# Kernel optimization log

Hardware: AMD Instinct MI355X
Metric: run time of the kernel (lower is better)

Reference implementation:

```python
import jax, jax.numpy as jnp
import numpy as np

N = 100000      # nodes
E = 1600000     # edges
IN, HG, HM, OUT = 512, 64, 64, 20


def _glorot(key, fan_in, fan_out):
    lim = 1.0 / np.sqrt(fan_in)
    return jax.random.uniform(key, (fan_in, fan_out), jnp.float32, -lim, lim)


def setup_inputs() -> dict:
    key = jax.random.key(0)
    ks = jax.random.split(key, 16)
    inp = {
        "x": jax.random.normal(ks[0], (N, IN), jnp.float32),
        "edge_index": jax.random.randint(ks[1], (2, E), 0, N, jnp.int64),
        "edge_attrs": jax.random.uniform(ks[2], (E,), jnp.float32),
        # GCNConv weights (PyG: x @ W then aggregate, + bias)
        "gc0_w": _glorot(ks[3], IN, HG), "gc0_b": jnp.zeros((HG,), jnp.float32),
        "gc1_w": _glorot(ks[4], HG, HG), "gc1_b": jnp.zeros((HG,), jnp.float32),
        "lin0_w": _glorot(ks[5], HG, HM), "lin0_b": jnp.zeros((HM,), jnp.float32),
        "lin1_w": _glorot(ks[6], HM, HM), "lin1_b": jnp.zeros((HM,), jnp.float32),
        "lin2_w": _glorot(ks[7], HM, HM), "lin2_b": jnp.zeros((HM,), jnp.float32),
        "lin3_w": _glorot(ks[8], HM, OUT), "lin3_b": jnp.zeros((OUT,), jnp.float32),
    }
    return inp


def _gcn_norm(edge_index, edge_attrs):
    # Add self loops (weight 1), compute symmetric normalization D^-1/2 A D^-1/2
    loop = jnp.arange(N, dtype=edge_index.dtype)
    row = jnp.concatenate([edge_index[0], loop])
    col = jnp.concatenate([edge_index[1], loop])
    w = jnp.concatenate([edge_attrs, jnp.ones((N,), edge_attrs.dtype)])
    deg = jax.ops.segment_sum(w, col, num_segments=N)
    dinv = jnp.where(deg > 0, jax.lax.rsqrt(jnp.maximum(deg, 1e-30)), 0.0)
    norm = dinv[row] * w * dinv[col]
    return row, col, norm


def _gcn_conv(x, W, b, row, col, norm):
    xw = x @ W                                   # [N, H]
    msg = norm[:, None] * xw[row]                # [E+N, H]
    return jax.ops.segment_sum(msg, col, num_segments=N) + b


def reference(x, edge_index, edge_attrs,
              gc0_w, gc0_b, gc1_w, gc1_b,
              lin0_w, lin0_b, lin1_w, lin1_b, lin2_w, lin2_b, lin3_w, lin3_b):
    row, col, norm = _gcn_norm(edge_index, edge_attrs)
    h = jax.nn.selu(_gcn_conv(x, gc0_w, gc0_b, row, col, norm))
    h = jax.nn.selu(_gcn_conv(h, gc1_w, gc1_b, row, col, norm))
    h = jax.nn.selu(h @ lin0_w + lin0_b)
    h = jax.nn.selu(h @ lin1_w + lin1_b)
    h = jax.nn.selu(h @ lin2_w + lin2_b)
    return jax.nn.softmax(h @ lin3_w + lin3_b, axis=-1)
```

## Files before the change

kernel.cpp:

```cpp
#include <hip/hip_runtime.h>
#include <math.h>

#define IN_DIM 512
#define HG 64
#define OUT_DIM 20

typedef __attribute__((ext_vector_type(8))) short bf16x8;
typedef __attribute__((ext_vector_type(4))) float f32x4;

__device__ __forceinline__ float selu_f(float x) {
    const float a = 1.6732632423543772f;
    const float s = 1.0507009873554805f;
    return x > 0.f ? s * x : s * a * expm1f(x);
}

__device__ __forceinline__ unsigned short f2bf(float f) {
    unsigned int u = __float_as_uint(f);
    u += 0x7FFFu + ((u >> 16) & 1u);
    return (unsigned short)(u >> 16);
}
__device__ __forceinline__ float bf2f(unsigned short b) {
    return __uint_as_float(((unsigned int)b) << 16);
}


__global__ void k_init(float* deg, int* cnt, int n) {
    int i = blockIdx.x * 256 + threadIdx.x;
    if (i < n) { deg[i] = 1.0f; cnt[i] = 0; }
}

__global__ void k_edgedeg(const int* __restrict__ ei, const float* __restrict__ ea,
                          float* deg, int* cnt, int E) {
    int e = blockIdx.x * 256 + threadIdx.x;
    if (e >= E) return;
    int c = ei[E + e];
    atomicAdd(&deg[c], ea[e]);
    atomicAdd(&cnt[c], 1);
}

__global__ void k_rsqrt(float* deg, int n) {
    int i = blockIdx.x * 256 + threadIdx.x;
    if (i < n) { float d = deg[i]; deg[i] = d > 0.f ? 1.0f / sqrtf(d) : 0.f; }
}

__device__ __forceinline__ int block_excl_scan(int v, int tid, int* wsum, int nw, int* total_out) {
    int lane = tid & 63, wv = tid >> 6;
    int incl = v;
    #pragma unroll
    for (int s = 1; s < 64; s <<= 1) {
        int t = __shfl_up(incl, s, 64);
        if (lane >= s) incl += t;
    }
    if (lane == 63) wsum[wv] = incl;
    __syncthreads();
    int prefix = 0;
    for (int i = 0; i < wv; i++) prefix += wsum[i];
    int total = 0;
    for (int i = 0; i < nw; i++) total += wsum[i];
    *total_out = total;
    return prefix + incl - v;
}

__global__ void k_scan1(const int* __restrict__ cnt, int* __restrict__ offar,
                        int* __restrict__ blockSums, int n) {
    __shared__ int wsum[4];
    int i = blockIdx.x * 256 + threadIdx.x;
    int v = (i < n) ? cnt[i] : 0;
    int total;
    int excl = block_excl_scan(v, threadIdx.x, wsum, 4, &total);
    if (i < n) offar[i] = excl;
    if (threadIdx.x == 0) blockSums[blockIdx.x] = total;
}

__global__ void k_scan2(const int* __restrict__ blockSums, int* __restrict__ blockOffs, int nb) {
    __shared__ int wsum[8];
    int v = (threadIdx.x < nb) ? blockSums[threadIdx.x] : 0;
    int total;
    int excl = block_excl_scan(v, threadIdx.x, wsum, 8, &total);
    if (threadIdx.x < nb) blockOffs[threadIdx.x] = excl;
}

__global__ void k_scan3(int* __restrict__ offar, const int* __restrict__ blockOffs,
                        int* __restrict__ cursor, int n, int E) {
    int i = blockIdx.x * 256 + threadIdx.x;
    if (i < n) {
        int o = offar[i] + blockOffs[blockIdx.x];
        offar[i] = o;
        cursor[i] = o;
    }
    if (i == 0) offar[n] = E;
}

__global__ void k_scatter(const int* __restrict__ ei, const float* __restrict__ ea,
                          const float* __restrict__ dinv, int* cursor,
                          int* __restrict__ srcA, float* __restrict__ valA, int E) {
    int e = blockIdx.x * 256 + threadIdx.x;
    if (e >= E) return;
    int r = ei[e], c = ei[E + e];
    int pos = atomicAdd(&cursor[c], 1);
    srcA[pos] = r;
    valA[pos] = dinv[r] * ea[e] * dinv[c];
}


__global__ void k_splitw(const float* __restrict__ W, unsigned short* __restrict__ hi,
                         unsigned short* __restrict__ lo, int K, int C, int Cpad) {
    int i = blockIdx.x * 256 + threadIdx.x;
    if (i >= Cpad * K) return;
    int c = i / K, k = i - c * K;
    float wv = (c < C) ? W[(size_t)k * C + c] : 0.f;
    unsigned short h = f2bf(wv);
    hi[i] = h;
    lo[i] = f2bf(wv - bf2f(h));
}


template <int K, bool BIAS, bool ACT>
__global__ __launch_bounds__(256, 3)
void k_gemm_mfma(const float* __restrict__ A, const unsigned short* __restrict__ WThi,
                 const unsigned short* __restrict__ WTlo, const float* __restrict__ bias,
                 float* __restrict__ out, int n) {
    const int t = threadIdx.x;
    const int lane = t & 63;
    const int w = t >> 6;
    const int l15 = lane & 15;
    const int g = lane >> 4;
    const int r0 = blockIdx.x * 128 + w * 32;
    if (r0 >= n) return;

    f32x4 acc[2][4];
    #pragma unroll
    for (int rt = 0; rt < 2; rt++)
        #pragma unroll
        for (int ct = 0; ct < 4; ct++) acc[rt][ct] = (f32x4)0.f;

    #pragma unroll 1
    for (int k0 = 0; k0 < K; k0 += 32) {
        bf16x8 bh[4], bl[4];
        #pragma unroll
        for (int ct = 0; ct < 4; ct++) {
            size_t off = (size_t)(ct * 16 + l15) * K + k0 + 8 * g;
            bh[ct] = *(const bf16x8*)(WThi + off);
            bl[ct] = *(const bf16x8*)(WTlo + off);
        }
        #pragma unroll
        for (int rt = 0; rt < 2; rt++) {
            const float* ap = A + (size_t)(r0 + rt * 16 + l15) * K + k0 + 8 * g;
            float4 v0 = *(const float4*)(ap);
            float4 v1 = *(const float4*)(ap + 4);
            float vv[8] = {v0.x, v0.y, v0.z, v0.w, v1.x, v1.y, v1.z, v1.w};
            bf16x8 ah, al;
            #pragma unroll
            for (int j = 0; j < 8; j++) {
                unsigned short h = f2bf(vv[j]);
                ah[j] = (short)h;
                al[j] = (short)f2bf(vv[j] - bf2f(h));
            }
            #pragma unroll
            for (int ct = 0; ct < 4; ct++) {
                acc[rt][ct] = __builtin_amdgcn_mfma_f32_16x16x32_bf16(ah, bh[ct], acc[rt][ct], 0, 0, 0);
                acc[rt][ct] = __builtin_amdgcn_mfma_f32_16x16x32_bf16(ah, bl[ct], acc[rt][ct], 0, 0, 0);
                acc[rt][ct] = __builtin_amdgcn_mfma_f32_16x16x32_bf16(al, bh[ct], acc[rt][ct], 0, 0, 0);
            }
        }
    }

    float bv[4];
    #pragma unroll
    for (int ct = 0; ct < 4; ct++) bv[ct] = BIAS ? bias[ct * 16 + l15] : 0.f;

    #pragma unroll
    for (int rt = 0; rt < 2; rt++) {
        #pragma unroll
        for (int r = 0; r < 4; r++) {
            int gr = r0 + rt * 16 + 4 * g + r;
            #pragma unroll
            for (int ct = 0; ct < 4; ct++) {
                float v = acc[rt][ct][r] + bv[ct];
                if (ACT) v = selu_f(v);
                out[(size_t)gr * 64 + ct * 16 + l15] = v;
            }
        }
    }
}


__global__ __launch_bounds__(256, 3)
void k_lin3s(const float* __restrict__ A, const unsigned short* __restrict__ WThi,
             const unsigned short* __restrict__ WTlo, const float* __restrict__ b3,
             float* __restrict__ out, int n) {
    const int t = threadIdx.x;
    const int lane = t & 63;
    const int w = t >> 6;
    const int l15 = lane & 15;
    const int g = lane >> 4;
    const int r0 = blockIdx.x * 128 + w * 32;
    if (r0 >= n) return;

    f32x4 acc[2][2];
    #pragma unroll
    for (int rt = 0; rt < 2; rt++)
        #pragma unroll
        for (int ct = 0; ct < 2; ct++) acc[rt][ct] = (f32x4)0.f;

    #pragma unroll 1
    for (int k0 = 0; k0 < 64; k0 += 32) {
        bf16x8 bh[2], bl[2];
        #pragma unroll
        for (int ct = 0; ct < 2; ct++) {
            size_t off = (size_t)(ct * 16 + l15) * 64 + k0 + 8 * g;
            bh[ct] = *(const bf16x8*)(WThi + off);
            bl[ct] = *(const bf16x8*)(WTlo + off);
        }
        #pragma unroll
        for (int rt = 0; rt < 2; rt++) {
            const float* ap = A + (size_t)(r0 + rt * 16 + l15) * 64 + k0 + 8 * g;
            float4 v0 = *(const float4*)(ap);
            float4 v1 = *(const float4*)(ap + 4);
            float vv[8] = {v0.x, v0.y, v0.z, v0.w, v1.x, v1.y, v1.z, v1.w};
            bf16x8 ah, al;
            #pragma unroll
            for (int j = 0; j < 8; j++) {
                unsigned short h = f2bf(vv[j]);
                ah[j] = (short)h;
                al[j] = (short)f2bf(vv[j] - bf2f(h));
            }
            #pragma unroll
            for (int ct = 0; ct < 2; ct++) {
                acc[rt][ct] = __builtin_amdgcn_mfma_f32_16x16x32_bf16(ah, bh[ct], acc[rt][ct], 0, 0, 0);
                acc[rt][ct] = __builtin_amdgcn_mfma_f32_16x16x32_bf16(ah, bl[ct], acc[rt][ct], 0, 0, 0);
                acc[rt][ct] = __builtin_amdgcn_mfma_f32_16x16x32_bf16(al, bh[ct], acc[rt][ct], 0, 0, 0);
            }
        }
    }

    float b0v = b3[l15];
    float b1v = (l15 < 4) ? b3[16 + l15] : 0.f;

    #pragma unroll
    for (int rt = 0; rt < 2; rt++) {
        #pragma unroll
        for (int r = 0; r < 4; r++) {
            int gr = r0 + rt * 16 + 4 * g + r;
            float v0 = acc[rt][0][r] + b0v;
            float v1 = (l15 < 4) ? acc[rt][1][r] + b1v : -INFINITY;
            float mx = fmaxf(v0, v1);
            mx = fmaxf(mx, __shfl_xor(mx, 1));
            mx = fmaxf(mx, __shfl_xor(mx, 2));
            mx = fmaxf(mx, __shfl_xor(mx, 4));
            mx = fmaxf(mx, __shfl_xor(mx, 8));
            float e0 = expf(v0 - mx);
            float e1 = (l15 < 4) ? expf(v1 - mx) : 0.f;
            float s = e0 + e1;
            s += __shfl_xor(s, 1);
            s += __shfl_xor(s, 2);
            s += __shfl_xor(s, 4);
            s += __shfl_xor(s, 8);
            float inv = 1.0f / s;
            out[(size_t)gr * OUT_DIM + l15] = e0 * inv;
            if (l15 < 4) out[(size_t)gr * OUT_DIM + 16 + l15] = e1 * inv;
        }
    }
}


__global__ __launch_bounds__(256) void k_agg(const float* __restrict__ xw, const float* __restrict__ dinv,
                                             const int* __restrict__ off, const int* __restrict__ srcA,
                                             const float* __restrict__ valA, const float* __restrict__ bias,
                                             float* __restrict__ out, int n) {
    int node = (blockIdx.x * 256 + threadIdx.x) >> 6;
    int lane = threadIdx.x & 63;
    if (node >= n) return;
    float d = dinv[node];
    float acc = d * d * xw[(size_t)node * 64 + lane];
    int p0 = off[node], p1 = off[node + 1];
    for (int p = p0; p < p1; ++p) {
        int s = srcA[p];
        float v = valA[p];
        acc += v * xw[(size_t)s * 64 + lane];
    }
    out[(size_t)node * 64 + lane] = selu_f(acc + bias[lane]);
}


extern "C" void kernel_launch(void* const* d_in, const int* in_sizes, int n_in,
                              void* d_out, int out_size, void* d_ws, size_t ws_size,
                              hipStream_t stream) {
    const float* x     = (const float*)d_in[0];
    const int*   ei    = (const int*)d_in[1];
    const float* ea    = (const float*)d_in[2];
    const float* gc0_w = (const float*)d_in[3];
    const float* gc0_b = (const float*)d_in[4];
    const float* gc1_w = (const float*)d_in[5];
    const float* gc1_b = (const float*)d_in[6];
    const float* lin0_w = (const float*)d_in[7];
    const float* lin0_b = (const float*)d_in[8];
    const float* lin1_w = (const float*)d_in[9];
    const float* lin1_b = (const float*)d_in[10];
    const float* lin2_w = (const float*)d_in[11];
    const float* lin2_b = (const float*)d_in[12];
    const float* lin3_w = (const float*)d_in[13];
    const float* lin3_b = (const float*)d_in[14];
    float* out = (float*)d_out;

    const int N = in_sizes[0] / IN_DIM;
    const int E = in_sizes[2];
    const int nb1 = (N + 255) / 256;

    char* w = (char*)d_ws;
    auto alloc = [&](size_t bytes) { char* p = w; w += (bytes + 255) & ~(size_t)255; return p; };
    float* dinv      = (float*)alloc((size_t)N * 4);
    int*   cnt       = (int*)alloc((size_t)N * 4);
    int*   offar     = (int*)alloc((size_t)(N + 1) * 4);
    int*   cursor    = (int*)alloc((size_t)N * 4);
    int*   blockSums = (int*)alloc((size_t)nb1 * 4);
    int*   blockOffs = (int*)alloc((size_t)nb1 * 4);
    int*   srcA      = (int*)alloc((size_t)E * 4);
    float* valA      = (float*)alloc((size_t)E * 4);
    float* bufA      = (float*)alloc((size_t)N * 64 * 4);
    float* bufB      = (float*)alloc((size_t)N * 64 * 4);
    unsigned short* wt0h = (unsigned short*)alloc(64 * 512 * 2);
    unsigned short* wt0l = (unsigned short*)alloc(64 * 512 * 2);
    unsigned short* wt1h = (unsigned short*)alloc(64 * 64 * 2);
    unsigned short* wt1l = (unsigned short*)alloc(64 * 64 * 2);
    unsigned short* wl0h = (unsigned short*)alloc(64 * 64 * 2);
    unsigned short* wl0l = (unsigned short*)alloc(64 * 64 * 2);
    unsigned short* wl1h = (unsigned short*)alloc(64 * 64 * 2);
    unsigned short* wl1l = (unsigned short*)alloc(64 * 64 * 2);
    unsigned short* wl2h = (unsigned short*)alloc(64 * 64 * 2);
    unsigned short* wl2l = (unsigned short*)alloc(64 * 64 * 2);
    unsigned short* wt3h = (unsigned short*)alloc(32 * 64 * 2);
    unsigned short* wt3l = (unsigned short*)alloc(32 * 64 * 2);

    const int gN = (N + 255) / 256;
    const int gE = (E + 255) / 256;
    const int gT = (N + 127) / 128;
    const int gA = (N + 3) / 4;

    k_init<<<gN, 256, 0, stream>>>(dinv, cnt, N);
    k_edgedeg<<<gE, 256, 0, stream>>>(ei, ea, dinv, cnt, E);
    k_rsqrt<<<gN, 256, 0, stream>>>(dinv, N);
    k_scan1<<<nb1, 256, 0, stream>>>(cnt, offar, blockSums, N);
    k_scan2<<<1, 512, 0, stream>>>(blockSums, blockOffs, nb1);
    k_scan3<<<nb1, 256, 0, stream>>>(offar, blockOffs, cursor, N, E);
    k_scatter<<<gE, 256, 0, stream>>>(ei, ea, dinv, cursor, srcA, valA, E);

    k_splitw<<<128, 256, 0, stream>>>(gc0_w, wt0h, wt0l, 512, 64, 64);
    k_splitw<<<16, 256, 0, stream>>>(gc1_w, wt1h, wt1l, 64, 64, 64);
    k_splitw<<<16, 256, 0, stream>>>(lin0_w, wl0h, wl0l, 64, 64, 64);
    k_splitw<<<16, 256, 0, stream>>>(lin1_w, wl1h, wl1l, 64, 64, 64);
    k_splitw<<<16, 256, 0, stream>>>(lin2_w, wl2h, wl2l, 64, 64, 64);
    k_splitw<<<8, 256, 0, stream>>>(lin3_w, wt3h, wt3l, 64, OUT_DIM, 32);

    k_gemm_mfma<IN_DIM, false, false><<<gT, 256, 0, stream>>>(x, wt0h, wt0l, nullptr, bufA, N);
    k_agg<<<gA, 256, 0, stream>>>(bufA, dinv, offar, srcA, valA, gc0_b, bufB, N);
    k_gemm_mfma<HG, false, false><<<gT, 256, 0, stream>>>(bufB, wt1h, wt1l, nullptr, bufA, N);
    k_agg<<<gA, 256, 0, stream>>>(bufA, dinv, offar, srcA, valA, gc1_b, bufB, N);
    k_gemm_mfma<HG, true, true><<<gT, 256, 0, stream>>>(bufB, wl0h, wl0l, lin0_b, bufA, N);
    k_gemm_mfma<HG, true, true><<<gT, 256, 0, stream>>>(bufA, wl1h, wl1l, lin1_b, bufB, N);
    k_gemm_mfma<HG, true, true><<<gT, 256, 0, stream>>>(bufB, wl2h, wl2l, lin2_b, bufA, N);
    k_lin3s<<<gT, 256, 0, stream>>>(bufA, wt3h, wt3l, lin3_b, out, N);
}
```

Measured before the change: 1.013 ms.

## Fuse dense MLP stack into one register-resident kernel; vectorize aggregation

The three hidden linear layers and the final linear+softmax are merged into one kernel. Activations stay in registers as split-bf16 MFMA operands, computed in transposed form so each layer's output feeds the next layer's B operand, which removes three round trips of a 100k×64 fp32 buffer through global memory. Separately, the aggregation kernel now has each wavefront handle a node with two half-waves over alternating edges, loading float2 per lane and unrolling by four to raise memory-level parallelism. The fused kernel adds register pressure, and the lin3 weight reads for padded rows 20-31 depend on how that buffer was sized.

```diff
diff --git a/kernel.cpp b/kernel.cpp
--- a/kernel.cpp
+++ b/kernel.cpp
@@ -6,6 +6,7 @@
 #define OUT_DIM 20
 
 typedef __attribute__((ext_vector_type(8))) short bf16x8;
+typedef __attribute__((ext_vector_type(4))) short bf16x4;
 typedef __attribute__((ext_vector_type(4))) float f32x4;
 
 __device__ __forceinline__ float selu_f(float x) {
@@ -185,85 +186,6 @@
 }
 
 
-__global__ __launch_bounds__(256, 3)
-void k_lin3s(const float* __restrict__ A, const unsigned short* __restrict__ WThi,
-             const unsigned short* __restrict__ WTlo, const float* __restrict__ b3,
-             float* __restrict__ out, int n) {
-    const int t = threadIdx.x;
-    const int lane = t & 63;
-    const int w = t >> 6;
-    const int l15 = lane & 15;
-    const int g = lane >> 4;
-    const int r0 = blockIdx.x * 128 + w * 32;
-    if (r0 >= n) return;
-
-    f32x4 acc[2][2];
-    #pragma unroll
-    for (int rt = 0; rt < 2; rt++)
-        #pragma unroll
-        for (int ct = 0; ct < 2; ct++) acc[rt][ct] = (f32x4)0.f;
-
-    #pragma unroll 1
-    for (int k0 = 0; k0 < 64; k0 += 32) {
-        bf16x8 bh[2], bl[2];
-        #pragma unroll
-        for (int ct = 0; ct < 2; ct++) {
-            size_t off = (size_t)(ct * 16 + l15) * 64 + k0 + 8 * g;
-            bh[ct] = *(const bf16x8*)(WThi + off);
-            bl[ct] = *(const bf16x8*)(WTlo + off);
-        }
-        #pragma unroll
-        for (int rt = 0; rt < 2; rt++) {
-            const float* ap = A + (size_t)(r0 + rt * 16 + l15) * 64 + k0 + 8 * g;
-            float4 v0 = *(const float4*)(ap);
-            float4 v1 = *(const float4*)(ap + 4);
-            float vv[8] = {v0.x, v0.y, v0.z, v0.w, v1.x, v1.y, v1.z, v1.w};
-            bf16x8 ah, al;
-            #pragma unroll
-            for (int j = 0; j < 8; j++) {
-                unsigned short h = f2bf(vv[j]);
-                ah[j] = (short)h;
-                al[j] = (short)f2bf(vv[j] - bf2f(h));
-            }
-            #pragma unroll
-            for (int ct = 0; ct < 2; ct++) {
-                acc[rt][ct] = __builtin_amdgcn_mfma_f32_16x16x32_bf16(ah, bh[ct], acc[rt][ct], 0, 0, 0);
-                acc[rt][ct] = __builtin_amdgcn_mfma_f32_16x16x32_bf16(ah, bl[ct], acc[rt][ct], 0, 0, 0);
-                acc[rt][ct] = __builtin_amdgcn_mfma_f32_16x16x32_bf16(al, bh[ct], acc[rt][ct], 0, 0, 0);
-            }
-        }
-    }
-
-    float b0v = b3[l15];
-    float b1v = (l15 < 4) ? b3[16 + l15] : 0.f;
-
-    #pragma unroll
-    for (int rt = 0; rt < 2; rt++) {
-        #pragma unroll
-        for (int r = 0; r < 4; r++) {
-            int gr = r0 + rt * 16 + 4 * g + r;
-            float v0 = acc[rt][0][r] + b0v;
-            float v1 = (l15 < 4) ? acc[rt][1][r] + b1v : -INFINITY;
-            float mx = fmaxf(v0, v1);
-            mx = fmaxf(mx, __shfl_xor(mx, 1));
-            mx = fmaxf(mx, __shfl_xor(mx, 2));
-            mx = fmaxf(mx, __shfl_xor(mx, 4));
-            mx = fmaxf(mx, __shfl_xor(mx, 8));
-            float e0 = expf(v0 - mx);
-            float e1 = (l15 < 4) ? expf(v1 - mx) : 0.f;
-            float s = e0 + e1;
-            s += __shfl_xor(s, 1);
-            s += __shfl_xor(s, 2);
-            s += __shfl_xor(s, 4);
-            s += __shfl_xor(s, 8);
-            float inv = 1.0f / s;
-            out[(size_t)gr * OUT_DIM + l15] = e0 * inv;
-            if (l15 < 4) out[(size_t)gr * OUT_DIM + 16 + l15] = e1 * inv;
-        }
-    }
-}
-
-
 __global__ __launch_bounds__(256) void k_agg(const float* __restrict__ xw, const float* __restrict__ dinv,
                                              const int* __restrict__ off, const int* __restrict__ srcA,
                                              const float* __restrict__ valA, const float* __restrict__ bias,
@@ -271,15 +193,196 @@
     int node = (blockIdx.x * 256 + threadIdx.x) >> 6;
     int lane = threadIdx.x & 63;
     if (node >= n) return;
-    float d = dinv[node];
-    float acc = d * d * xw[(size_t)node * 64 + lane];
+    const int half = lane >> 5;
+    const int l32 = lane & 31;
+    const float2* __restrict__ xw2 = (const float2*)xw;
+
     int p0 = off[node], p1 = off[node + 1];
-    for (int p = p0; p < p1; ++p) {
+    float ax = 0.f, ay = 0.f;
+    int p = p0 + half;
+    for (; p + 6 < p1; p += 8) {
+        int s0 = srcA[p];
+        int s1 = srcA[p + 2];
+        int s2 = srcA[p + 4];
+        int s3 = srcA[p + 6];
+        float v0 = valA[p], v1 = valA[p + 2], v2 = valA[p + 4], v3 = valA[p + 6];
+        float2 x0 = xw2[(size_t)s0 * 32 + l32];
+        float2 x1 = xw2[(size_t)s1 * 32 + l32];
+        float2 x2 = xw2[(size_t)s2 * 32 + l32];
+        float2 x3 = xw2[(size_t)s3 * 32 + l32];
+        ax += v0 * x0.x + v1 * x1.x + v2 * x2.x + v3 * x3.x;
+        ay += v0 * x0.y + v1 * x1.y + v2 * x2.y + v3 * x3.y;
+    }
+    for (; p < p1; p += 2) {
         int s = srcA[p];
         float v = valA[p];
-        acc += v * xw[(size_t)s * 64 + lane];
-    }
-    out[(size_t)node * 64 + lane] = selu_f(acc + bias[lane]);
+        float2 xv = xw2[(size_t)s * 32 + l32];
+        ax += v * xv.x;
+        ay += v * xv.y;
+    }
+    ax += __shfl_xor(ax, 32);
+    ay += __shfl_xor(ay, 32);
+    if (half == 0) {
+        float d = dinv[node];
+        float2 self = xw2[(size_t)node * 32 + l32];
+        float2 o;
+        o.x = selu_f(ax + d * d * self.x + bias[2 * l32]);
+        o.y = selu_f(ay + d * d * self.y + bias[2 * l32 + 1]);
+        ((float2*)out)[(size_t)node * 32 + l32] = o;
+    }
+}
+
+
+__global__ __launch_bounds__(256, 3)
+void k_dense(const float* __restrict__ H,
+             const unsigned short* __restrict__ w0h, const unsigned short* __restrict__ w0l, const float* __restrict__ b0,
+             const unsigned short* __restrict__ w1h, const unsigned short* __restrict__ w1l, const float* __restrict__ b1,
+             const unsigned short* __restrict__ w2h, const unsigned short* __restrict__ w2l, const float* __restrict__ b2,
+             const unsigned short* __restrict__ w3h, const unsigned short* __restrict__ w3l, const float* __restrict__ b3,
+             float* __restrict__ out, int n) {
+    const int t = threadIdx.x, lane = t & 63, w = t >> 6;
+    const int l15 = lane & 15, g = lane >> 4;
+    const int r0 = blockIdx.x * 128 + w * 32;
+    if (r0 >= n) return;
+
+    bf16x8 bh[2][2], bl[2][2];
+    #pragma unroll
+    for (int nt = 0; nt < 2; nt++) {
+        const float* hp = H + (size_t)(r0 + nt * 16 + l15) * 64;
+        #pragma unroll
+        for (int k0 = 0; k0 < 2; k0++) {
+            float4 c0 = *(const float4*)(hp + 32 * k0 + 4 * g);
+            float4 c1 = *(const float4*)(hp + 32 * k0 + 16 + 4 * g);
+            float vv[8] = {c0.x, c0.y, c0.z, c0.w, c1.x, c1.y, c1.z, c1.w};
+            #pragma unroll
+            for (int j = 0; j < 8; j++) {
+                unsigned short hb = f2bf(vv[j]);
+                bh[nt][k0][j] = (short)hb;
+                bl[nt][k0][j] = (short)f2bf(vv[j] - bf2f(hb));
+            }
+        }
+    }
+
+    const unsigned short* whs[3] = {w0h, w1h, w2h};
+    const unsigned short* wls[3] = {w0l, w1l, w2l};
+    const float* bs[3] = {b0, b1, b2};
+
+    #pragma unroll
+    for (int layer = 0; layer < 3; layer++) {
+        float accS[2][4][4];
+        #pragma unroll
+        for (int ct = 0; ct < 4; ct++) {
+            bf16x8 ah[2], al[2];
+            #pragma unroll
+            for (int k0 = 0; k0 < 2; k0++) {
+                size_t off = (size_t)(16 * ct + l15) * 64 + 32 * k0 + 4 * g;
+                bf16x4 h0 = *(const bf16x4*)(whs[layer] + off);
+                bf16x4 h1 = *(const bf16x4*)(whs[layer] + off + 16);
+                bf16x4 l0 = *(const bf16x4*)(wls[layer] + off);
+                bf16x4 l1 = *(const bf16x4*)(wls[layer] + off + 16);
+                #pragma unroll
+                for (int j = 0; j < 4; j++) {
+                    ah[k0][j] = h0[j]; ah[k0][4 + j] = h1[j];
+                    al[k0][j] = l0[j]; al[k0][4 + j] = l1[j];
+                }
+            }
+            float4 bv = *(const float4*)(bs[layer] + 16 * ct + 4 * g);
+            float bvr[4] = {bv.x, bv.y, bv.z, bv.w};
+            #pragma unroll
+            for (int nt = 0; nt < 2; nt++) {
+                f32x4 acc = (f32x4)0.f;
+                #pragma unroll
+                for (int k0 = 0; k0 < 2; k0++) {
+                    acc = __builtin_amdgcn_mfma_f32_16x16x32_bf16(ah[k0], bh[nt][k0], acc, 0, 0, 0);
+                    acc = __builtin_amdgcn_mfma_f32_16x16x32_bf16(ah[k0], bl[nt][k0], acc, 0, 0, 0);
+                    acc = __builtin_amdgcn_mfma_f32_16x16x32_bf16(al[k0], bh[nt][k0], acc, 0, 0, 0);
+                }
+                #pragma unroll
+                for (int r = 0; r < 4; r++) accS[nt][ct][r] = selu_f(acc[r] + bvr[r]);
+            }
+        }
+        #pragma unroll
+        for (int nt = 0; nt < 2; nt++)
+            #pragma unroll
+            for (int k0 = 0; k0 < 2; k0++)
+                #pragma unroll
+                for (int j = 0; j < 8; j++) {
+                    float v = accS[nt][2 * k0 + (j >> 2)][j & 3];
+                    unsigned short hb = f2bf(v);
+                    bh[nt][k0][j] = (short)hb;
+                    bl[nt][k0][j] = (short)f2bf(v - bf2f(hb));
+                }
+    }
+
+    float z[2][2][4];
+    #pragma unroll
+    for (int ct = 0; ct < 2; ct++) {
+        bf16x8 ah[2], al[2];
+        #pragma unroll
+        for (int k0 = 0; k0 < 2; k0++) {
+            size_t off = (size_t)(16 * ct + l15) * 64 + 32 * k0 + 4 * g;
+            bf16x4 h0 = *(const bf16x4*)(w3h + off);
+            bf16x4 h1 = *(const bf16x4*)(w3h + off + 16);
+            bf16x4 l0 = *(const bf16x4*)(w3l + off);
+            bf16x4 l1 = *(const bf16x4*)(w3l + off + 16);
+            #pragma unroll
+            for (int j = 0; j < 4; j++) {
+                ah[k0][j] = h0[j]; ah[k0][4 + j] = h1[j];
+                al[k0][j] = l0[j]; al[k0][4 + j] = l1[j];
+            }
+        }
+        #pragma unroll
+        for (int nt = 0; nt < 2; nt++) {
+            f32x4 acc = (f32x4)0.f;
+            #pragma unroll
+            for (int k0 = 0; k0 < 2; k0++) {
+                acc = __builtin_amdgcn_mfma_f32_16x16x32_bf16(ah[k0], bh[nt][k0], acc, 0, 0, 0);
+                acc = __builtin_amdgcn_mfma_f32_16x16x32_bf16(ah[k0], bl[nt][k0], acc, 0, 0, 0);
+                acc = __builtin_amdgcn_mfma_f32_16x16x32_bf16(al[k0], bh[nt][k0], acc, 0, 0, 0);
+            }
+            #pragma unroll
+            for (int r = 0; r < 4; r++) {
+                int f = 16 * ct + 4 * g + r;
+                float bb = (f < OUT_DIM) ? b3[f] : 0.f;
+                z[nt][ct][r] = acc[r] + bb;
+            }
+        }
+    }
+    #pragma unroll
+    for (int nt = 0; nt < 2; nt++) {
+        int node = r0 + nt * 16 + l15;
+        float mx = -INFINITY;
+        #pragma unroll
+        for (int ct = 0; ct < 2; ct++)
+            #pragma unroll
+            for (int r = 0; r < 4; r++) {
+                if (ct == 0 || g == 0) mx = fmaxf(mx, z[nt][ct][r]);
+            }
+        mx = fmaxf(mx, __shfl_xor(mx, 16));
+        mx = fmaxf(mx, __shfl_xor(mx, 32));
+        float e[2][4];
+        float s = 0.f;
+        #pragma unroll
+        for (int ct = 0; ct < 2; ct++)
+            #pragma unroll
+            for (int r = 0; r < 4; r++) {
+                if (ct == 0 || g == 0) {
+                    e[ct][r] = expf(z[nt][ct][r] - mx);
+                    s += e[ct][r];
+                } else e[ct][r] = 0.f;
+            }
+        s += __shfl_xor(s, 16);
+        s += __shfl_xor(s, 32);
+        float inv = 1.0f / s;
+        #pragma unroll
+        for (int ct = 0; ct < 2; ct++)
+            #pragma unroll
+            for (int r = 0; r < 4; r++) {
+                int f = 16 * ct + 4 * g + r;
+                if (ct == 0 || g == 0)
+                    out[(size_t)node * OUT_DIM + f] = e[ct][r] * inv;
+            }
+    }
 }
 
 
@@ -356,8 +459,10 @@
     k_agg<<<gA, 256, 0, stream>>>(bufA, dinv, offar, srcA, valA, gc0_b, bufB, N);
     k_gemm_mfma<HG, false, false><<<gT, 256, 0, stream>>>(bufB, wt1h, wt1l, nullptr, bufA, N);
     k_agg<<<gA, 256, 0, stream>>>(bufA, dinv, offar, srcA, valA, gc1_b, bufB, N);
-    k_gemm_mfma<HG, true, true><<<gT, 256, 0, stream>>>(bufB, wl0h, wl0l, lin0_b, bufA, N);
-    k_gemm_mfma<HG, true, true><<<gT, 256, 0, stream>>>(bufA, wl1h, wl1l, lin1_b, bufB, N);
-    k_gemm_mfma<HG, true, true><<<gT, 256, 0, stream>>>(bufB, wl2h, wl2l, lin2_b, bufA, N);
-    k_lin3s<<<gT, 256, 0, stream>>>(bufA, wt3h, wt3l, lin3_b, out, N);
-}
+    k_dense<<<gT, 256, 0, stream>>>(bufB,
+                                    wl0h, wl0l, lin0_b,
+                                    wl1h, wl1l, lin1_b,
+                                    wl2h, wl2l, lin2_b,
+                                    wt3h, wt3l, lin3_b,
+                                    out, N);
+}
```

After: 833.7 us. 17.7% less time.
